# Optimization experiments

Hardware: AMD Instinct MI355X
Metric: run time of the kernel (lower is better)

The kernel has to match this reference:

```python
import jax, jax.numpy as jnp
import numpy as np

T, B, N, GH, GW, ENC, H, D, TH = 16, 512, 8192, 3, 13, 128, 4, 32, 64
G = GH * GW          # 39 social grid cells
EMB = H * D          # 128 = n_head * att_out
SCALE = 1.0 / np.sqrt(ENC).astype(np.float32)
LN_EPS = 1e-5


def lstm(x, Wih, Whh, bih, bhh):
    # x: [T, Batch, in] -> hidden states [T, Batch, ENC]; torch gate order i,f,g,o
    n = x.shape[1]
    h0 = jnp.zeros((n, ENC), x.dtype)

    def step(carry, xt):
        h, c = carry
        g = xt @ Wih.T + bih + h @ Whh.T + bhh
        i, f, gg, o = jnp.split(g, 4, axis=-1)
        c = jax.nn.sigmoid(f) * c + jax.nn.sigmoid(i) * jnp.tanh(gg)
        h = jax.nn.sigmoid(o) * jnp.tanh(c)
        return (h, c), h

    _, hs = jax.lax.scan(step, (h0, h0), x)
    return hs


def glu(x, Wa, ba, Wg, bg):
    return (x @ Wa.T + ba) * jax.nn.sigmoid(x @ Wg.T + bg)


def layer_norm(x, g, b):
    m = jnp.mean(x, -1, keepdims=True)
    v = jnp.var(x, -1, keepdims=True)
    return (x - m) * jax.lax.rsqrt(v + LN_EPS) * g + b


def setup_inputs():
    key = jax.random.key(0)
    ks = jax.random.split(key, 40)

    def rn(i, sh, s=1.0):
        return jax.random.normal(ks[i], sh, jnp.float32) * s

    inp = {
        'hist': rn(0, (T, B, 2)), 'nbrs': rn(1, (T, N, 2)),
        'va': rn(2, (T, B, 2)), 'nbrsva': rn(3, (T, N, 2)),
        'lane': jnp.zeros((T, B, 1), jnp.float32),
        'nbrslane': jnp.zeros((T, N, 1), jnp.float32),
        'cls': rn(4, (T, B, 1)), 'nbrscls': rn(5, (T, N, 1)),
    }
    # boolean social-grid mask with exactly N true cells (cell-level, full enc dim)
    rng = np.random.default_rng(0)
    flat = np.zeros(B * G, bool)
    flat[rng.permutation(B * G)[:N]] = True
    inp['mask'] = jnp.asarray(np.broadcast_to(flat.reshape(B, GH, GW, 1), (B, GH, GW, ENC)))

    s = 0.05
    inp.update({
        'W1': rn(6, (TH, 5), s), 'b1': jnp.zeros((TH,), jnp.float32),
        'Wih': rn(7, (4 * ENC, TH), s), 'Whh': rn(8, (4 * ENC, ENC), s),
        'bih': jnp.zeros((4 * ENC,), jnp.float32), 'bhh': jnp.zeros((4 * ENC,), jnp.float32),
        'Wq': rn(9, (EMB, ENC), s), 'bq': jnp.zeros((EMB,), jnp.float32),
        'Wk': rn(10, (EMB, ENC), s), 'bk': jnp.zeros((EMB,), jnp.float32),
        'Wv': rn(11, (EMB, ENC), s), 'bv': jnp.zeros((EMB,), jnp.float32),
        'Wg1a': rn(12, (ENC, EMB), s), 'bg1a': jnp.zeros((ENC,), jnp.float32),
        'Wg1g': rn(13, (ENC, EMB), s), 'bg1g': jnp.zeros((ENC,), jnp.float32),
        'Wqt': rn(14, (EMB, ENC), s), 'bqt': jnp.zeros((EMB,), jnp.float32),
        'Wkt': rn(15, (EMB, ENC), s), 'bkt': jnp.zeros((EMB,), jnp.float32),
        'Wvt': rn(16, (EMB, ENC), s), 'bvt': jnp.zeros((EMB,), jnp.float32),
        'Wg2a': rn(17, (ENC, EMB), s), 'bg2a': jnp.zeros((ENC,), jnp.float32),
        'Wg2g': rn(18, (ENC, EMB), s), 'bg2g': jnp.zeros((ENC,), jnp.float32),
        'ln_g': jnp.ones((ENC,), jnp.float32), 'ln_b': jnp.zeros((ENC,), jnp.float32),
    })
    return inp


def reference(hist, nbrs, mask, va, nbrsva, lane, nbrslane, cls, nbrscls,
              W1, b1, Wih, Whh, bih, bhh, Wq, bq, Wk, bk, Wv, bv,
              Wg1a, bg1a, Wg1g, bg1g, Wqt, bqt, Wkt, bkt, Wvt, bvt,
              Wg2a, bg2a, Wg2g, bg2g, ln_g, ln_b):
    # f_length == 5 branch
    hist_in = jnp.concatenate((hist, cls, va), -1)        # [T,B,5]
    nbrs_in = jnp.concatenate((nbrs, nbrscls, nbrsva), -1)  # [T,N,5]

    hist_enc = jax.nn.elu(hist_in @ W1.T + b1)
    hist_h = lstm(hist_enc, Wih, Whh, bih, bhh)           # [T,B,ENC]
    hist_hidden = jnp.transpose(hist_h, (1, 0, 2))        # [B,T,ENC]

    nbrs_enc = jax.nn.elu(nbrs_in @ W1.T + b1)
    nbrs_h = lstm(nbrs_enc, Wih, Whh, bih, bhh)           # [T,N,ENC]

    # masked_scatter: fill true grid cells (row-major over B*G) with neighbor states
    cell = mask[:, :, :, 0].reshape(B * G)                # [B*G] bool
    idx = jnp.cumsum(cell.astype(jnp.int32)) - 1          # position among true cells
    gathered = nbrs_h[:, jnp.clip(idx, 0, N - 1), :]      # [T,B*G,ENC]
    soc = jnp.where(cell[None, :, None], gathered, 0.0).reshape(T, B, G, ENC)

    # spatial multi-head attention (each timestep attends over its own grid)
    q = (hist_hidden @ Wq.T + bq).reshape(B, T, H, D)
    k = (soc @ Wk.T + bk).reshape(T, B, G, H, D)
    v = (soc @ Wv.T + bv).reshape(T, B, G, H, D)
    a = jax.nn.softmax(jnp.einsum('bthd,tbghd->bthg', q, k) * SCALE, -1)
    spa = jnp.einsum('bthg,tbghd->bthd', a, v).reshape(B, T, EMB)
    spa = glu(spa, Wg1a, bg1a, Wg1g, bg1g)

    values = layer_norm(hist_hidden + spa, ln_g, ln_b)    # [B,T,ENC]

    # temporal multi-head attention over T
    qt = (values @ Wqt.T + bqt).reshape(B, T, H, D)
    kt = (values @ Wkt.T + bkt).reshape(B, T, H, D)
    vt = (values @ Wvt.T + bvt).reshape(B, T, H, D)
    at = jax.nn.softmax(jnp.einsum('bthd,bshd->bhts', qt, kt) * SCALE, -1)
    tmp = jnp.einsum('bhts,bshd->bthd', at, vt).reshape(B, T, EMB)
    tmp = glu(tmp, Wg2a, bg2a, Wg2g, bg2g)

    # use_spatial=True
    return layer_norm(hist_hidden + spa + tmp, ln_g, ln_b)
```

## Files before the change

### kernel.cpp

```cpp
#include <hip/hip_runtime.h>
#include <math.h>

#define T_ 16
#define B_ 512
#define N_ 8192
#define G_ 39
#define ENC_ 128
#define TH_ 64
#define MROWS 8704
#define GATE 512
#define KCAT 192
#define SCALE_ 0.08838834764831845f
#define LNEPS 1e-5f
#define NBLK 136

typedef short bf16x8 __attribute__((ext_vector_type(8)));
typedef float f32x4  __attribute__((ext_vector_type(4)));

__device__ __forceinline__ float sigm(float x){ return 1.0f/(1.0f+expf(-x)); }
__device__ __forceinline__ float rcpf(float x){ return __builtin_amdgcn_rcpf(x); }
__device__ __forceinline__ float sigm_f(float x){ return rcpf(1.0f + __expf(-x)); }
__device__ __forceinline__ float tanh_f(float x){ return 1.0f - 2.0f*rcpf(__expf(2.0f*x) + 1.0f); }
__device__ __forceinline__ unsigned short f2bf(float f){
  unsigned int u = __float_as_uint(f);
  unsigned int r = u + 0x7FFFu + ((u>>16)&1u);
  return (unsigned short)(r>>16);
}
__device__ __forceinline__ float bf2f(unsigned short h){
  return __uint_as_float(((unsigned int)h)<<16);
}

__global__ __launch_bounds__(256) void k_prep(
    const float* __restrict__ Wih, const float* __restrict__ Whh,
    const float* __restrict__ bih, const float* __restrict__ bhh,
    const float* __restrict__ Wk,  const float* __restrict__ bk,
    const float* __restrict__ Wv,  const float* __restrict__ bv,
    const float* __restrict__ Wq,
    const float* __restrict__ Wqt, const float* __restrict__ bqt,
    const float* __restrict__ Wkt, const float* __restrict__ bkt,
    const float* __restrict__ Wvt, const float* __restrict__ bvt,
    const float* __restrict__ Wg1a, const float* __restrict__ bg1a,
    const float* __restrict__ Wg1g, const float* __restrict__ bg1g,
    const float* __restrict__ Wg2a, const float* __restrict__ bg2a,
    const float* __restrict__ Wg2g, const float* __restrict__ bg2g,
    unsigned short* __restrict__ WcatB, float* __restrict__ biasg,
    unsigned short* __restrict__ WkvB,  float* __restrict__ bkv,
    unsigned short* __restrict__ WqB,
    unsigned short* __restrict__ WqktB, float* __restrict__ bqkt,
    unsigned short* __restrict__ Wg1B,  float* __restrict__ bg1,
    unsigned short* __restrict__ Wg2B,  float* __restrict__ bg2)
{
  int i = blockIdx.x*256 + threadIdx.x;
  if (i < GATE*KCAT) {
    int n = i / KCAT, k = i % KCAT;
    WcatB[i] = f2bf((k < TH_) ? Wih[n*TH_ + k] : Whh[n*ENC_ + (k - TH_)]);
  }
  if (i < GATE) biasg[i] = bih[i] + bhh[i];
  if (i < 2*ENC_*ENC_) {
    int n = i >> 7, k = i & 127;
    WkvB[i] = f2bf((n < ENC_) ? Wk[n*ENC_ + k] : Wv[(n-ENC_)*ENC_ + k]);
    Wg1B[i] = f2bf((n < ENC_) ? Wg1a[n*ENC_ + k] : Wg1g[(n-ENC_)*ENC_ + k]);
    Wg2B[i] = f2bf((n < ENC_) ? Wg2a[n*ENC_ + k] : Wg2g[(n-ENC_)*ENC_ + k]);
  }
  if (i < 2*ENC_) {
    bkv[i] = (i < ENC_) ? bk[i] : bv[i-ENC_];
    bg1[i] = (i < ENC_) ? bg1a[i] : bg1g[i-ENC_];
    bg2[i] = (i < ENC_) ? bg2a[i] : bg2g[i-ENC_];
  }
  if (i < ENC_*ENC_) WqB[i] = f2bf(Wq[i]);
  if (i < 3*ENC_*ENC_) {
    int n = i >> 7, k = i & 127;
    float w = (n < ENC_) ? Wqt[n*ENC_ + k] : (n < 2*ENC_) ? Wkt[(n-ENC_)*ENC_ + k]
                                                          : Wvt[(n-2*ENC_)*ENC_ + k];
    WqktB[i] = f2bf(w);
  }
  if (i < 3*ENC_) bqkt[i] = (i < ENC_) ? bqt[i] : (i < 2*ENC_) ? bkt[i-ENC_] : bvt[i-2*ENC_];
}

__device__ __forceinline__ int cellval(const unsigned char* m, long cell, int w) {
  long byte = cell * 128L * w;
  if (w == 1) return m[byte] != 0;
  if (w == 2) return *(const unsigned short*)(m + byte) != 0;
  if (w == 4) return *(const unsigned int*)(m + byte) != 0;
  return *(const unsigned long long*)(m + byte) != 0ULL;
}
__device__ __forceinline__ int cellconsist(const unsigned char* m, long cell, int w) {
  long byte = cell * 128L * w;
  if (w == 1) { unsigned char v = m[byte];
    for (int j = 1; j < 8; ++j) if (m[byte + j] != v) return 0; return 1; }
  if (w == 2) { unsigned short v = *(const unsigned short*)(m + byte);
    for (int j = 1; j < 8; ++j) if (*(const unsigned short*)(m + byte + 2L*j) != v) return 0; return 1; }
  if (w == 4) { unsigned int v = *(const unsigned int*)(m + byte);
    for (int j = 1; j < 8; ++j) if (*(const unsigned int*)(m + byte + 4L*j) != v) return 0; return 1; }
  unsigned long long v = *(const unsigned long long*)(m + byte);
  for (int j = 1; j < 8; ++j) if (*(const unsigned long long*)(m + byte + 8L*j) != v) return 0; return 1;
}

__global__ void k_detect(const unsigned char* __restrict__ mask, int* __restrict__ wsel)
{
  __shared__ int bad;
  int tid = threadIdx.x;
  int chosen = 0;
  for (int w = 1; w <= 8 && !chosen; w <<= 1) {
    if (tid == 0) bad = 0;
    __syncthreads();
    int ok = 1;
    for (int c = tid; c < 512; c += 256) ok &= cellconsist(mask, c, w);
    if (!ok) bad = 1;
    __syncthreads();
    if (!bad) chosen = w;
    __syncthreads();
  }
  if (tid == 0) *wsel = chosen ? chosen : 1;
}

__global__ void k_count(const unsigned char* __restrict__ mask,
                        const int* __restrict__ wsel, int* __restrict__ bcnt)
{
  __shared__ int sc[256];
  int tid = threadIdx.x;
  long cell = (long)blockIdx.x*256 + tid;
  sc[tid] = cellval(mask, cell, *wsel);
  __syncthreads();
  for (int off = 128; off; off >>= 1) {
    if (tid < off) sc[tid] += sc[tid + off];
    __syncthreads();
  }
  if (tid == 0) bcnt[blockIdx.x] = sc[0];
}

__global__ void k_fill(const unsigned char* __restrict__ mask,
                       const int* __restrict__ wsel, const int* __restrict__ bcnt,
                       int* __restrict__ nidx)
{
  __shared__ int sc[256];
  int tid = threadIdx.x, blk = blockIdx.x;
  long cell = (long)blk*256 + tid;
  int on = cellval(mask, cell, *wsel);
  sc[tid] = on;
  __syncthreads();
  for (int off = 1; off < 256; off <<= 1) {
    int v = (tid >= off) ? sc[tid - off] : 0;
    __syncthreads();
    sc[tid] += v;
    __syncthreads();
  }
  int base = 0;
  for (int i = 0; i < blk; ++i) base += bcnt[i];
  nidx[cell] = on ? (base + sc[tid] - 1) : -1;
}

struct AP {
  const float *hist, *cls, *va, *nbrs, *nbrscls, *nbrsva;
  const float *W1, *b1;
  const unsigned short *Wcat, *Wkv, *Wq;
  const float *biasg, *bkv, *bq;
  float *hh;
  float *qbuf;
  unsigned short *knvB;
  unsigned short *Hsp;
  float *csp;
  int c0, tch;
};

__global__ __launch_bounds__(512, 2) void k_lstm(AP p)
{
  __shared__ unsigned short Hl[2*64*128];
  __shared__ unsigned short Xl[64*64];
  __shared__ float finl[16][64][5];

  const int tid = threadIdx.x;
  const int w = tid >> 6, l = tid & 63;
  const int lr = l & 15, lk = (l >> 4) * 8, lq = (l >> 4) * 4;
  const int bi = blockIdx.x, bm = bi * 64;
  const bool ish = (bi < 8);

  bf16x8 wg[4][6];
  #pragma unroll
  for (int g = 0; g < 4; ++g)
    #pragma unroll
    for (int ks = 0; ks < 6; ++ks)
      wg[g][ks] = *(const bf16x8*)(p.Wcat + (long)(g*128 + w*16 + lr)*KCAT + ks*32 + lk);

  const int ch = w*16 + lr;
  const float bgi = p.biasg[ch], bgf = p.biasg[128+ch],
              bgg = p.biasg[256+ch], bgo = p.biasg[384+ch];

  const float w1c0 = p.W1[l*5+0], w1c1 = p.W1[l*5+1], w1c2 = p.W1[l*5+2],
              w1c3 = p.W1[l*5+3], w1c4 = p.W1[l*5+4], b1c = p.b1[l];

  for (int idx = tid; idx < p.tch*320; idx += 512) {
    int t4 = idx / 320, rem = idx - t4*320;
    int row = rem / 5, f = rem - row*5;
    long r = ish ? ((long)(p.c0 + t4)*B_ + bm + row) : ((long)(p.c0 + t4)*N_ + (bm - B_) + row);
    const float* ph = ish ? p.hist : p.nbrs;
    const float* pc = ish ? p.cls  : p.nbrscls;
    const float* pv = ish ? p.va   : p.nbrsva;
    finl[t4][row][f] = (f < 2) ? ph[r*2 + f] : (f == 2) ? pc[r] : pv[r*2 + (f-3)];
  }

  float creg[4][4];
  if (p.c0 == 0) {
    for (int i = tid; i < 64*128; i += 512) Hl[i] = 0;
    #pragma unroll
    for (int mi = 0; mi < 4; ++mi)
      #pragma unroll
      for (int q = 0; q < 4; ++q) creg[mi][q] = 0.0f;
  } else {
    for (int i = tid; i < 64*128; i += 512) Hl[i] = p.Hsp[(long)bm*128 + i];
    #pragma unroll
    for (int mi = 0; mi < 4; ++mi)
      #pragma unroll
      for (int q = 0; q < 4; ++q) creg[mi][q] = p.csp[((long)bi*512 + tid)*16 + mi*4 + q];
  }
  __syncthreads();

  int cur = 0;
  for (int tl = 0; tl < p.tch; ++tl) {
    int t = p.c0 + tl;
    {
      #pragma unroll
      for (int j = 0; j < 8; ++j) {
        int row = w*8 + j;
        float s = b1c + finl[tl][row][0]*w1c0 + finl[tl][row][1]*w1c1
                      + finl[tl][row][2]*w1c2 + finl[tl][row][3]*w1c3
                      + finl[tl][row][4]*w1c4;
        s = (s > 0.0f) ? s : expm1f(s);
        Xl[row*64 + (l ^ ((row & 7) << 3))] = f2bf(s);
      }
    }
    __syncthreads();
    f32x4 acc[4][4] = {};
    #pragma unroll
    for (int ks = 0; ks < 2; ++ks) {
      bf16x8 a[4];
      #pragma unroll
      for (int mi = 0; mi < 4; ++mi) {
        int row = mi*16 + lr;
        int col = (ks*32 + lk) ^ ((row & 7) << 3);
        a[mi] = *(const bf16x8*)(Xl + row*64 + col);
      }
      #pragma unroll
      for (int g = 0; g < 4; ++g)
        #pragma unroll
        for (int mi = 0; mi < 4; ++mi)
          acc[g][mi] = __builtin_amdgcn_mfma_f32_16x16x32_bf16(a[mi], wg[g][ks], acc[g][mi], 0, 0, 0);
    }
    #pragma unroll
    for (int ks = 0; ks < 4; ++ks) {
      bf16x8 a[4];
      #pragma unroll
      for (int mi = 0; mi < 4; ++mi) {
        int row = mi*16 + lr;
        int col = (ks*32 + lk) ^ ((row & 7) << 3);
        a[mi] = *(const bf16x8*)(Hl + cur*8192 + row*128 + col);
      }
      #pragma unroll
      for (int g = 0; g < 4; ++g)
        #pragma unroll
        for (int mi = 0; mi < 4; ++mi)
          acc[g][mi] = __builtin_amdgcn_mfma_f32_16x16x32_bf16(a[mi], wg[g][2+ks], acc[g][mi], 0, 0, 0);
    }
    int nxt = cur ^ 1;
    #pragma unroll
    for (int mi = 0; mi < 4; ++mi)
      #pragma unroll
      for (int q = 0; q < 4; ++q) {
        int row = mi*16 + lq + q;
        float gi = acc[0][mi][q] + bgi;
        float gf = acc[1][mi][q] + bgf;
        float gg = acc[2][mi][q] + bgg;
        float go = acc[3][mi][q] + bgo;
        float cc = sigm_f(gf)*creg[mi][q] + sigm_f(gi)*tanh_f(gg);
        creg[mi][q] = cc;
        float hv = sigm_f(go)*tanh_f(cc);
        Hl[nxt*8192 + row*128 + (ch ^ ((row & 7) << 3))] = f2bf(hv);
        if (ish) p.hh[((long)(bm + row)*T_ + t)*128 + ch] = hv;
      }
    __syncthreads();
    cur = nxt;
    if (!ish) {
      f32x4 a2[4][2] = {};
      #pragma unroll
      for (int ks = 0; ks < 4; ++ks) {
        bf16x8 a[4];
        #pragma unroll
        for (int mi = 0; mi < 4; ++mi) {
          int row = mi*16 + lr;
          int col = (ks*32 + lk) ^ ((row & 7) << 3);
          a[mi] = *(const bf16x8*)(Hl + cur*8192 + row*128 + col);
        }
        #pragma unroll
        for (int ni = 0; ni < 2; ++ni) {
          bf16x8 b = *(const bf16x8*)(p.Wkv + (long)(w*32 + ni*16 + lr)*128 + ks*32 + lk);
          #pragma unroll
          for (int mi = 0; mi < 4; ++mi)
            a2[mi][ni] = __builtin_amdgcn_mfma_f32_16x16x32_bf16(a[mi], b, a2[mi][ni], 0, 0, 0);
        }
      }
      long nr = bm - B_;
      #pragma unroll
      for (int mi = 0; mi < 4; ++mi)
        #pragma unroll
        for (int ni = 0; ni < 2; ++ni) {
          int c2 = w*32 + ni*16 + lr;
          float bb = p.bkv[c2];
          #pragma unroll
          for (int q = 0; q < 4; ++q)
            p.knvB[((long)tl*N_ + nr + mi*16 + lq + q)*256 + c2] = f2bf(a2[mi][ni][q] + bb);
        }
    } else {
      f32x4 a2[4] = {};
      #pragma unroll
      for (int ks = 0; ks < 4; ++ks) {
        bf16x8 a[4];
        #pragma unroll
        for (int mi = 0; mi < 4; ++mi) {
          int row = mi*16 + lr;
          int col = (ks*32 + lk) ^ ((row & 7) << 3);
          a[mi] = *(const bf16x8*)(Hl + cur*8192 + row*128 + col);
        }
        bf16x8 b = *(const bf16x8*)(p.Wq + (long)(w*16 + lr)*128 + ks*32 + lk);
        #pragma unroll
        for (int mi = 0; mi < 4; ++mi)
          a2[mi] = __builtin_amdgcn_mfma_f32_16x16x32_bf16(a[mi], b, a2[mi], 0, 0, 0);
      }
      float bb = p.bq[ch];
      #pragma unroll
      for (int mi = 0; mi < 4; ++mi)
        #pragma unroll
        for (int q = 0; q < 4; ++q)
          p.qbuf[((long)t*B_ + bm + mi*16 + lq + q)*128 + ch] = a2[mi][q] + bb;
    }
    __syncthreads();
  }
  for (int i = tid; i < 64*128; i += 512) p.Hsp[(long)bm*128 + i] = Hl[cur*8192 + i];
  #pragma unroll
  for (int mi = 0; mi < 4; ++mi)
    #pragma unroll
    for (int q = 0; q < 4; ++q)
      p.csp[((long)bi*512 + tid)*16 + mi*4 + q] = creg[mi][q];
}

__global__ __launch_bounds__(256) void k_attn_sp(
    int c0, int ltch,
    const float* __restrict__ qbuf, const unsigned short* __restrict__ knvB,
    const float* __restrict__ bk, const float* __restrict__ bv,
    const int* __restrict__ nidx, unsigned short* __restrict__ spaB)
{
  int tid = threadIdx.x;
  int w = tid >> 6, l = tid & 63;
  __shared__ int sn[4][G_];
  __shared__ float aw[4][4][40];
  int gwid = blockIdx.x*4 + w;
  int b = gwid >> ltch;
  int tl = gwid & ((1 << ltch) - 1);
  int t = c0 + tl;
  if (l < G_) sn[w][l] = nidx[b*G_ + l];
  __syncthreads();
  float qA = qbuf[((long)t*B_ + b)*128 + l];
  float qB = qbuf[((long)t*B_ + b)*128 + 64 + l];
  for (int g = 0; g < G_; ++g) {
    int ni = sn[w][g];
    const unsigned short* kr = knvB + ((long)tl*N_ + ni)*256;
    float kA = (ni >= 0) ? bf2f(kr[l])      : bk[l];
    float kB = (ni >= 0) ? bf2f(kr[64 + l]) : bk[64 + l];
    float pA = qA*kA, pB = qB*kB;
    pA += __shfl_xor(pA, 16); pA += __shfl_xor(pA, 8); pA += __shfl_xor(pA, 4);
    pA += __shfl_xor(pA, 2);  pA += __shfl_xor(pA, 1);
    pB += __shfl_xor(pB, 16); pB += __shfl_xor(pB, 8); pB += __shfl_xor(pB, 4);
    pB += __shfl_xor(pB, 2);  pB += __shfl_xor(pB, 1);
    if ((l & 31) == 0) {
      int hb = l >> 5;
      aw[w][hb][g]     = pA * SCALE_;
      aw[w][2+hb][g]   = pB * SCALE_;
    }
  }
  __syncthreads();
  int hA = l >> 5, hB = 2 + (l >> 5);
  float mxA = -1e30f, mxB = -1e30f;
  for (int g = 0; g < G_; ++g) {
    mxA = fmaxf(mxA, aw[w][hA][g]);
    mxB = fmaxf(mxB, aw[w][hB][g]);
  }
  float sA = 0.f, sB = 0.f, oA = 0.f, oB = 0.f;
  for (int g = 0; g < G_; ++g) {
    int ni = sn[w][g];
    const unsigned short* vr = knvB + ((long)tl*N_ + ni)*256 + 128;
    float vA = (ni >= 0) ? bf2f(vr[l])      : bv[l];
    float vB = (ni >= 0) ? bf2f(vr[64 + l]) : bv[64 + l];
    float eA = expf(aw[w][hA][g] - mxA);
    float eB = expf(aw[w][hB][g] - mxB);
    sA += eA; sB += eB; oA += eA*vA; oB += eB*vB;
  }
  spaB[((long)b*T_ + t)*128 + l]      = f2bf(oA / sA);
  spaB[((long)b*T_ + t)*128 + 64 + l] = f2bf(oB / sB);
}

__global__ __launch_bounds__(256) void k_gemm_bf16(
    const unsigned short* __restrict__ A, int lda,
    const unsigned short* __restrict__ W, int ldw,
    const float* __restrict__ bias,
    float* __restrict__ C, int ldc, int K)
{
  int tid = threadIdx.x;
  int w = tid >> 6, l = tid & 63;
  int lr = l & 15, lk = (l >> 4) * 8, lq = (l >> 4) * 4;
  int bm = blockIdx.x * 64;
  int bn = blockIdx.y * 128 + w * 32;
  f32x4 acc[4][2] = {};
  for (int k0 = 0; k0 < K; k0 += 32) {
    bf16x8 a[4], b[2];
    #pragma unroll
    for (int mi = 0; mi < 4; ++mi)
      a[mi] = *(const bf16x8*)(A + (long)(bm + mi*16 + lr)*lda + k0 + lk);
    #pragma unroll
    for (int ni = 0; ni < 2; ++ni)
      b[ni] = *(const bf16x8*)(W + (long)(bn + ni*16 + lr)*ldw + k0 + lk);
    #pragma unroll
    for (int mi = 0; mi < 4; ++mi)
      #pragma unroll
      for (int ni = 0; ni < 2; ++ni)
        acc[mi][ni] = __builtin_amdgcn_mfma_f32_16x16x32_bf16(a[mi], b[ni], acc[mi][ni], 0, 0, 0);
  }
  #pragma unroll
  for (int mi = 0; mi < 4; ++mi)
    #pragma unroll
    for (int ni = 0; ni < 2; ++ni) {
      int col = bn + ni*16 + lr;
      float bb = bias[col];
      #pragma unroll
      for (int q = 0; q < 4; ++q)
        C[(long)(bm + mi*16 + lq + q)*ldc + col] = acc[mi][ni][q] + bb;
    }
}

__global__ __launch_bounds__(256) void k_gemm_bf16o(
    const unsigned short* __restrict__ A, int lda,
    const unsigned short* __restrict__ W, int ldw,
    const float* __restrict__ bias,
    unsigned short* __restrict__ C, int ldc, int K)
{
  int tid = threadIdx.x;
  int w = tid >> 6, l = tid & 63;
  int lr = l & 15, lk = (l >> 4) * 8, lq = (l >> 4) * 4;
  int bm = blockIdx.x * 64;
  int bn = blockIdx.y * 128 + w * 32;
  f32x4 acc[4][2] = {};
  for (int k0 = 0; k0 < K; k0 += 32) {
    bf16x8 a[4], b[2];
    #pragma unroll
    for (int mi = 0; mi < 4; ++mi)
      a[mi] = *(const bf16x8*)(A + (long)(bm + mi*16 + lr)*lda + k0 + lk);
    #pragma unroll
    for (int ni = 0; ni < 2; ++ni)
      b[ni] = *(const bf16x8*)(W + (long)(bn + ni*16 + lr)*ldw + k0 + lk);
    #pragma unroll
    for (int mi = 0; mi < 4; ++mi)
      #pragma unroll
      for (int ni = 0; ni < 2; ++ni)
        acc[mi][ni] = __builtin_amdgcn_mfma_f32_16x16x32_bf16(a[mi], b[ni], acc[mi][ni], 0, 0, 0);
  }
  #pragma unroll
  for (int mi = 0; mi < 4; ++mi)
    #pragma unroll
    for (int ni = 0; ni < 2; ++ni) {
      int col = bn + ni*16 + lr;
      float bb = bias[col];
      #pragma unroll
      for (int q = 0; q < 4; ++q)
        C[(long)(bm + mi*16 + lq + q)*ldc + col] = f2bf(acc[mi][ni][q] + bb);
    }
}

__global__ __launch_bounds__(256) void k_glu_addln(
    const float* __restrict__ t12, const float* __restrict__ res,
    const float* __restrict__ lg, const float* __restrict__ lb,
    float* __restrict__ sum_out, unsigned short* __restrict__ ln_bf16,
    float* __restrict__ ln_f32)
{
  int gtid = blockIdx.x*256 + threadIdx.x;
  int r = gtid >> 6;
  int l = threadIdx.x & 63;
  if (r >= B_*T_) return;
  long b4 = (long)r*256, b2 = (long)r*128;
  float xA = res[b2 + l]      + t12[b4 + l]      * sigm(t12[b4 + 128 + l]);
  float xB = res[b2 + 64 + l] + t12[b4 + 64 + l] * sigm(t12[b4 + 192 + l]);
  if (sum_out) { sum_out[b2 + l] = xA; sum_out[b2 + 64 + l] = xB; }
  float s = xA + xB, s2 = xA*xA + xB*xB;
  #pragma unroll
  for (int off = 32; off; off >>= 1) { s += __shfl_xor(s, off); s2 += __shfl_xor(s2, off); }
  float mean = s * (1.0f/128.0f);
  float var  = s2 * (1.0f/128.0f) - mean*mean;
  float inv  = rsqrtf(var + LNEPS);
  float oA = (xA - mean)*inv*lg[l]      + lb[l];
  float oB = (xB - mean)*inv*lg[64 + l] + lb[64 + l];
  if (ln_bf16) { ln_bf16[b2 + l] = f2bf(oA); ln_bf16[b2 + 64 + l] = f2bf(oB); }
  if (ln_f32)  { ln_f32[b2 + l] = oA;        ln_f32[b2 + 64 + l] = oB; }
}

__global__ __launch_bounds__(128) void k_attn_t(
    const unsigned short* __restrict__ qkt, unsigned short* __restrict__ out)
{
  int b = blockIdx.x, tid = threadIdx.x;
  __shared__ float sq[16][128], sk[16][128], sv[16][128];
  __shared__ float sc[16][4][16];
  for (int i = tid; i < T_*ENC_; i += 128) {
    int tt = i >> 7, j = i & 127;
    long a = ((long)b*T_ + tt)*384;
    sq[tt][j] = bf2f(qkt[a + j]);
    sk[tt][j] = bf2f(qkt[a + 128 + j]);
    sv[tt][j] = bf2f(qkt[a + 256 + j]);
  }
  __syncthreads();
  for (int e = tid; e < 1024; e += 128) {
    int t = e >> 6, s = (e >> 2) & 15, h2 = e & 3;
    float pp = 0.0f;
    #pragma unroll
    for (int d2 = 0; d2 < 32; ++d2) pp += sq[t][h2*32 + d2] * sk[s][h2*32 + d2];
    sc[t][h2][s] = pp * SCALE_;
  }
  __syncthreads();
  if (tid < 64) {
    int t = tid >> 2, h2 = tid & 3;
    float mx = -1e30f;
    for (int s = 0; s < 16; ++s) mx = fmaxf(mx, sc[t][h2][s]);
    float sum = 0.0f;
    for (int s = 0; s < 16; ++s) { float e2 = expf(sc[t][h2][s] - mx); sc[t][h2][s] = e2; sum += e2; }
    float inv = 1.0f / sum;
    for (int s = 0; s < 16; ++s) sc[t][h2][s] *= inv;
  }
  __syncthreads();
  int h2 = tid >> 5, d2 = tid & 31;
  for (int t = 0; t < 16; ++t) {
    float acc = 0.0f;
    for (int s = 0; s < 16; ++s) acc += sc[t][h2][s] * sv[s][h2*32 + d2];
    out[((long)b*T_ + t)*128 + tid] = f2bf(acc);
  }
}

extern "C" void kernel_launch(void* const* d_in, const int* in_sizes, int n_in,
                              void* d_out, int out_size, void* d_ws, size_t ws_size,
                              hipStream_t stream)
{
  const float* hist    = (const float*)d_in[0];
  const float* nbrs    = (const float*)d_in[1];
  const float* va      = (const float*)d_in[2];
  const float* nbrsva  = (const float*)d_in[3];
  const float* cls     = (const float*)d_in[6];
  const float* nbrscls = (const float*)d_in[7];
  const unsigned char* mask = (const unsigned char*)d_in[8];
  const float* W1  = (const float*)d_in[9];
  const float* b1  = (const float*)d_in[10];
  const float* Wih = (const float*)d_in[11];
  const float* Whh = (const float*)d_in[12];
  const float* bih = (const float*)d_in[13];
  const float* bhh = (const float*)d_in[14];
  const float* Wq  = (const float*)d_in[15];
  const float* bq  = (const float*)d_in[16];
  const float* Wk  = (const float*)d_in[17];
  const float* bk  = (const float*)d_in[18];
  const float* Wv  = (const float*)d_in[19];
  const float* bv  = (const float*)d_in[20];
  const float* Wg1a = (const float*)d_in[21];
  const float* bg1a = (const float*)d_in[22];
  const float* Wg1g = (const float*)d_in[23];
  const float* bg1g = (const float*)d_in[24];
  const float* Wqt = (const float*)d_in[25];
  const float* bqt = (const float*)d_in[26];
  const float* Wkt = (const float*)d_in[27];
  const float* bkt = (const float*)d_in[28];
  const float* Wvt = (const float*)d_in[29];
  const float* bvt = (const float*)d_in[30];
  const float* Wg2a = (const float*)d_in[31];
  const float* bg2a = (const float*)d_in[32];
  const float* Wg2g = (const float*)d_in[33];
  const float* bg2g = (const float*)d_in[34];
  const float* ln_g = (const float*)d_in[35];
  const float* ln_b = (const float*)d_in[36];

  size_t fixed = 0;
  {
    size_t items[] = {
      (size_t)GATE*KCAT*2, (size_t)GATE*4, (size_t)2*ENC_*ENC_*2, (size_t)2*ENC_*4,
      (size_t)ENC_*ENC_*2, (size_t)3*ENC_*ENC_*2, (size_t)3*ENC_*4,
      (size_t)2*ENC_*ENC_*2, (size_t)2*ENC_*4, (size_t)2*ENC_*ENC_*2, (size_t)2*ENC_*4,
      (size_t)B_*T_*ENC_*4,
      (size_t)T_*B_*ENC_*4,
      (size_t)MROWS*ENC_*2,
      (size_t)NBLK*512*16*4,
      (size_t)B_*T_*ENC_*2,
      (size_t)B_*T_*2*ENC_*4,
      (size_t)B_*T_*ENC_*4,
      (size_t)B_*T_*ENC_*2,
      (size_t)B_*T_*3*ENC_*2,
      (size_t)B_*T_*ENC_*2,
      (size_t)B_*G_*4, (size_t)78*4, (size_t)4
    };
    for (size_t v : items) fixed += (v + 255) & ~(size_t)255;
  }
  int tch = 16, ltch = 4;
  while (tch > 4 && fixed + ((size_t)tch*N_*256*2 + 255) > ws_size) { tch >>= 1; ltch--; }

  char* base = (char*)d_ws;
  size_t off = 0;
  auto alloc = [&](size_t bytes) { char* r = base + off; off = (off + bytes + 255) & ~(size_t)255; return r; };
  unsigned short* WcatB = (unsigned short*)alloc(GATE*KCAT*2);
  float*          biasg = (float*)alloc(GATE*4);
  unsigned short* WkvB  = (unsigned short*)alloc(2*ENC_*ENC_*2);
  float*          bkv   = (float*)alloc(2*ENC_*4);
  unsigned short* WqB   = (unsigned short*)alloc(ENC_*ENC_*2);
  unsigned short* WqktB = (unsigned short*)alloc(3*ENC_*ENC_*2);
  float*          bqkt  = (float*)alloc(3*ENC_*4);
  unsigned short* Wg1B  = (unsigned short*)alloc(2*ENC_*ENC_*2);
  float*          bg1   = (float*)alloc(2*ENC_*4);
  unsigned short* Wg2B  = (unsigned short*)alloc(2*ENC_*ENC_*2);
  float*          bg2   = (float*)alloc(2*ENC_*4);
  float*          hh    = (float*)alloc((size_t)B_*T_*ENC_*4);
  float*          qbuf  = (float*)alloc((size_t)T_*B_*ENC_*4);
  unsigned short* Hsp   = (unsigned short*)alloc((size_t)MROWS*ENC_*2);
  float*          csp   = (float*)alloc((size_t)NBLK*512*16*4);
  unsigned short* spaB  = (unsigned short*)alloc((size_t)B_*T_*ENC_*2);
  float*          t12   = (float*)alloc((size_t)B_*T_*2*ENC_*4);
  float*          S1    = (float*)alloc((size_t)B_*T_*ENC_*4);
  unsigned short* valsB = (unsigned short*)alloc((size_t)B_*T_*ENC_*2);
  unsigned short* qktB  = (unsigned short*)alloc((size_t)B_*T_*3*ENC_*2);
  unsigned short* atoB  = (unsigned short*)alloc((size_t)B_*T_*ENC_*2);
  int*            nidx  = (int*)alloc((size_t)B_*G_*4);
  int*            bcnt  = (int*)alloc(78*4);
  int*            wsel  = (int*)alloc(4);
  unsigned short* knvB  = (unsigned short*)alloc((size_t)tch*N_*256*2);

  k_prep<<<384, 256, 0, stream>>>(
      Wih, Whh, bih, bhh, Wk, bk, Wv, bv, Wq,
      Wqt, bqt, Wkt, bkt, Wvt, bvt,
      Wg1a, bg1a, Wg1g, bg1g, Wg2a, bg2a, Wg2g, bg2g,
      WcatB, biasg, WkvB, bkv, WqB, WqktB, bqkt, Wg1B, bg1, Wg2B, bg2);
  k_detect<<<1, 256, 0, stream>>>(mask, wsel);
  k_count<<<78, 256, 0, stream>>>(mask, wsel, bcnt);
  k_fill<<<78, 256, 0, stream>>>(mask, wsel, bcnt, nidx);

  AP ap;
  ap.hist = hist; ap.cls = cls; ap.va = va;
  ap.nbrs = nbrs; ap.nbrscls = nbrscls; ap.nbrsva = nbrsva;
  ap.W1 = W1; ap.b1 = b1;
  ap.Wcat = WcatB; ap.Wkv = WkvB; ap.Wq = WqB;
  ap.biasg = biasg; ap.bkv = bkv; ap.bq = bq;
  ap.hh = hh; ap.qbuf = qbuf; ap.knvB = knvB; ap.Hsp = Hsp; ap.csp = csp;
  ap.tch = tch;
  for (int c0 = 0; c0 < T_; c0 += tch) {
    ap.c0 = c0;
    k_lstm<<<NBLK, 512, 0, stream>>>(ap);
    k_attn_sp<<<(B_*tch)/4, 256, 0, stream>>>(c0, ltch, qbuf, knvB, bk, bv, nidx, spaB);
  }

  k_gemm_bf16<<<dim3((B_*T_)/64, 2), 256, 0, stream>>>(spaB, 128, Wg1B, 128, bg1, t12, 256, 128);
  k_glu_addln<<<(B_*T_*64)/256, 256, 0, stream>>>(t12, hh, ln_g, ln_b, S1, valsB, nullptr);
  k_gemm_bf16o<<<dim3((B_*T_)/64, 3), 256, 0, stream>>>(valsB, 128, WqktB, 128, bqkt, qktB, 384, 128);
  k_attn_t<<<B_, 128, 0, stream>>>(qktB, atoB);
  k_gemm_bf16<<<dim3((B_*T_)/64, 2), 256, 0, stream>>>(atoB, 128, Wg2B, 128, bg2, t12, 256, 128);
  k_glu_addln<<<(B_*T_*64)/256, 256, 0, stream>>>(t12, S1, ln_g, ln_b, nullptr, nullptr, (float*)d_out);
}
```

Measured before the change: 310.6 us.

## Fold K/V projections into query side and precompute encoder for all timesteps

Spatial attention no longer projects every neighbour hidden state to K and V. The query is multiplied by per-head block-diagonal Wk once per (b,t), and attention runs over raw bf16 neighbour hidden states. Wv is applied after aggregation, with per-head weighted hidden sums fed through a block-diagonal GEMM. The input encoder moves to a separate kernel that writes bf16 features for all timesteps, so the LSTM runs in one launch without chunking or state spill. The cost is storing all neighbour hidden states (T*N*128 bf16), LSTM weights read from global each step instead of held in registers, and occupancy lowered to one block per CU.

```diff
diff --git a/kernel.cpp b/kernel.cpp
--- a/kernel.cpp
+++ b/kernel.cpp
@@ -33,8 +33,7 @@
 __global__ __launch_bounds__(256) void k_prep(
     const float* __restrict__ Wih, const float* __restrict__ Whh,
     const float* __restrict__ bih, const float* __restrict__ bhh,
-    const float* __restrict__ Wk,  const float* __restrict__ bk,
-    const float* __restrict__ Wv,  const float* __restrict__ bv,
+    const float* __restrict__ Wk,  const float* __restrict__ Wv,
     const float* __restrict__ Wq,
     const float* __restrict__ Wqt, const float* __restrict__ bqt,
     const float* __restrict__ Wkt, const float* __restrict__ bkt,
@@ -44,8 +43,9 @@
     const float* __restrict__ Wg2a, const float* __restrict__ bg2a,
     const float* __restrict__ Wg2g, const float* __restrict__ bg2g,
     unsigned short* __restrict__ WcatB, float* __restrict__ biasg,
-    unsigned short* __restrict__ WkvB,  float* __restrict__ bkv,
     unsigned short* __restrict__ WqB,
+    unsigned short* __restrict__ WkD,  unsigned short* __restrict__ WvD,
+    float* __restrict__ zero512,
     unsigned short* __restrict__ WqktB, float* __restrict__ bqkt,
     unsigned short* __restrict__ Wg1B,  float* __restrict__ bg1,
     unsigned short* __restrict__ Wg2B,  float* __restrict__ bg2)
@@ -56,18 +56,27 @@
     WcatB[i] = f2bf((k < TH_) ? Wih[n*TH_ + k] : Whh[n*ENC_ + (k - TH_)]);
   }
   if (i < GATE) biasg[i] = bih[i] + bhh[i];
+  if (i < ENC_*ENC_) WqB[i] = f2bf(Wq[i]);
+  if (i < 512*128) {
+    int r = i >> 7, dc = i & 127;
+    int h = r >> 7, e = r & 127;
+    WkD[i] = ((dc >> 5) == h) ? f2bf(Wk[dc*128 + e]) : (unsigned short)0;
+  }
+  if (i < 128*512) {
+    int r = i >> 9, kk = i & 511;
+    int hp = kk >> 7, e = kk & 127;
+    WvD[i] = (hp == (r >> 5)) ? f2bf(Wv[r*128 + e]) : (unsigned short)0;
+  }
+  if (i < 512) zero512[i] = 0.0f;
   if (i < 2*ENC_*ENC_) {
     int n = i >> 7, k = i & 127;
-    WkvB[i] = f2bf((n < ENC_) ? Wk[n*ENC_ + k] : Wv[(n-ENC_)*ENC_ + k]);
     Wg1B[i] = f2bf((n < ENC_) ? Wg1a[n*ENC_ + k] : Wg1g[(n-ENC_)*ENC_ + k]);
     Wg2B[i] = f2bf((n < ENC_) ? Wg2a[n*ENC_ + k] : Wg2g[(n-ENC_)*ENC_ + k]);
   }
   if (i < 2*ENC_) {
-    bkv[i] = (i < ENC_) ? bk[i] : bv[i-ENC_];
     bg1[i] = (i < ENC_) ? bg1a[i] : bg1g[i-ENC_];
     bg2[i] = (i < ENC_) ? bg2a[i] : bg2g[i-ENC_];
   }
-  if (i < ENC_*ENC_) WqB[i] = f2bf(Wq[i]);
   if (i < 3*ENC_*ENC_) {
     int n = i >> 7, k = i & 127;
     float w = (n < ENC_) ? Wqt[n*ENC_ + k] : (n < 2*ENC_) ? Wkt[(n-ENC_)*ENC_ + k]
@@ -150,24 +159,39 @@
   nidx[cell] = on ? (base + sc[tid] - 1) : -1;
 }
 
+__global__ __launch_bounds__(256) void k_encode_all(
+    const float* __restrict__ hist, const float* __restrict__ cls, const float* __restrict__ va,
+    const float* __restrict__ nbrs, const float* __restrict__ nbrscls, const float* __restrict__ nbrsva,
+    const float* __restrict__ W1, const float* __restrict__ b1,
+    unsigned short* __restrict__ XencB)
+{
+  int i = blockIdx.x*256 + threadIdx.x;
+  int t = blockIdx.y;
+  int o = i & 63, m = i >> 6;
+  float in0, in1, in2, in3, in4;
+  if (m < B_) {
+    int r = t*B_ + m;
+    in0 = hist[r*2]; in1 = hist[r*2+1]; in2 = cls[r]; in3 = va[r*2]; in4 = va[r*2+1];
+  } else {
+    int r = t*N_ + (m - B_);
+    in0 = nbrs[r*2]; in1 = nbrs[r*2+1]; in2 = nbrscls[r]; in3 = nbrsva[r*2]; in4 = nbrsva[r*2+1];
+  }
+  const float* w = W1 + o*5;
+  float s = b1[o] + in0*w[0] + in1*w[1] + in2*w[2] + in3*w[3] + in4*w[4];
+  XencB[((long)t*MROWS + m)*64 + o] = f2bf((s > 0.0f) ? s : expm1f(s));
+}
+
 struct AP {
-  const float *hist, *cls, *va, *nbrs, *nbrscls, *nbrsva;
-  const float *W1, *b1;
-  const unsigned short *Wcat, *Wkv, *Wq;
-  const float *biasg, *bkv, *bq;
+  const unsigned short *Xenc, *Wcat, *Wq;
+  const float *biasg, *bq;
   float *hh;
-  float *qbuf;
-  unsigned short *knvB;
-  unsigned short *Hsp;
-  float *csp;
-  int c0, tch;
+  unsigned short *qB;
+  unsigned short *HnB;
 };
 
-__global__ __launch_bounds__(512, 2) void k_lstm(AP p)
+__global__ __launch_bounds__(512, 1) void k_lstm(AP p)
 {
   __shared__ unsigned short Hl[2*64*128];
-  __shared__ unsigned short Xl[64*64];
-  __shared__ float finl[16][64][5];
 
   const int tid = threadIdx.x;
   const int w = tid >> 6, l = tid & 63;
@@ -175,76 +199,42 @@
   const int bi = blockIdx.x, bm = bi * 64;
   const bool ish = (bi < 8);
 
-  bf16x8 wg[4][6];
+  bf16x8 wgh[4][4];
   #pragma unroll
   for (int g = 0; g < 4; ++g)
     #pragma unroll
-    for (int ks = 0; ks < 6; ++ks)
-      wg[g][ks] = *(const bf16x8*)(p.Wcat + (long)(g*128 + w*16 + lr)*KCAT + ks*32 + lk);
+    for (int ks = 0; ks < 4; ++ks)
+      wgh[g][ks] = *(const bf16x8*)(p.Wcat + (long)(g*128 + w*16 + lr)*KCAT + 64 + ks*32 + lk);
 
   const int ch = w*16 + lr;
   const float bgi = p.biasg[ch], bgf = p.biasg[128+ch],
               bgg = p.biasg[256+ch], bgo = p.biasg[384+ch];
-
-  const float w1c0 = p.W1[l*5+0], w1c1 = p.W1[l*5+1], w1c2 = p.W1[l*5+2],
-              w1c3 = p.W1[l*5+3], w1c4 = p.W1[l*5+4], b1c = p.b1[l];
-
-  for (int idx = tid; idx < p.tch*320; idx += 512) {
-    int t4 = idx / 320, rem = idx - t4*320;
-    int row = rem / 5, f = rem - row*5;
-    long r = ish ? ((long)(p.c0 + t4)*B_ + bm + row) : ((long)(p.c0 + t4)*N_ + (bm - B_) + row);
-    const float* ph = ish ? p.hist : p.nbrs;
-    const float* pc = ish ? p.cls  : p.nbrscls;
-    const float* pv = ish ? p.va   : p.nbrsva;
-    finl[t4][row][f] = (f < 2) ? ph[r*2 + f] : (f == 2) ? pc[r] : pv[r*2 + (f-3)];
-  }
-
+  const float bqv = ish ? p.bq[ch] : 0.0f;
+
+  for (int i = tid; i < 64*128; i += 512) Hl[i] = 0;
   float creg[4][4];
-  if (p.c0 == 0) {
-    for (int i = tid; i < 64*128; i += 512) Hl[i] = 0;
-    #pragma unroll
-    for (int mi = 0; mi < 4; ++mi)
-      #pragma unroll
-      for (int q = 0; q < 4; ++q) creg[mi][q] = 0.0f;
-  } else {
-    for (int i = tid; i < 64*128; i += 512) Hl[i] = p.Hsp[(long)bm*128 + i];
-    #pragma unroll
-    for (int mi = 0; mi < 4; ++mi)
-      #pragma unroll
-      for (int q = 0; q < 4; ++q) creg[mi][q] = p.csp[((long)bi*512 + tid)*16 + mi*4 + q];
-  }
+  #pragma unroll
+  for (int mi = 0; mi < 4; ++mi)
+    #pragma unroll
+    for (int q = 0; q < 4; ++q) creg[mi][q] = 0.0f;
   __syncthreads();
 
   int cur = 0;
-  for (int tl = 0; tl < p.tch; ++tl) {
-    int t = p.c0 + tl;
-    {
-      #pragma unroll
-      for (int j = 0; j < 8; ++j) {
-        int row = w*8 + j;
-        float s = b1c + finl[tl][row][0]*w1c0 + finl[tl][row][1]*w1c1
-                      + finl[tl][row][2]*w1c2 + finl[tl][row][3]*w1c3
-                      + finl[tl][row][4]*w1c4;
-        s = (s > 0.0f) ? s : expm1f(s);
-        Xl[row*64 + (l ^ ((row & 7) << 3))] = f2bf(s);
-      }
-    }
-    __syncthreads();
+  for (int t = 0; t < T_; ++t) {
     f32x4 acc[4][4] = {};
     #pragma unroll
     for (int ks = 0; ks < 2; ++ks) {
       bf16x8 a[4];
       #pragma unroll
-      for (int mi = 0; mi < 4; ++mi) {
-        int row = mi*16 + lr;
-        int col = (ks*32 + lk) ^ ((row & 7) << 3);
-        a[mi] = *(const bf16x8*)(Xl + row*64 + col);
-      }
-      #pragma unroll
-      for (int g = 0; g < 4; ++g)
+      for (int mi = 0; mi < 4; ++mi)
+        a[mi] = *(const bf16x8*)(p.Xenc + ((long)t*MROWS + bm + mi*16 + lr)*64 + ks*32 + lk);
+      #pragma unroll
+      for (int g = 0; g < 4; ++g) {
+        bf16x8 b = *(const bf16x8*)(p.Wcat + (long)(g*128 + w*16 + lr)*KCAT + ks*32 + lk);
         #pragma unroll
         for (int mi = 0; mi < 4; ++mi)
-          acc[g][mi] = __builtin_amdgcn_mfma_f32_16x16x32_bf16(a[mi], wg[g][ks], acc[g][mi], 0, 0, 0);
+          acc[g][mi] = __builtin_amdgcn_mfma_f32_16x16x32_bf16(a[mi], b, acc[g][mi], 0, 0, 0);
+      }
     }
     #pragma unroll
     for (int ks = 0; ks < 4; ++ks) {
@@ -259,7 +249,7 @@
       for (int g = 0; g < 4; ++g)
         #pragma unroll
         for (int mi = 0; mi < 4; ++mi)
-          acc[g][mi] = __builtin_amdgcn_mfma_f32_16x16x32_bf16(a[mi], wg[g][2+ks], acc[g][mi], 0, 0, 0);
+          acc[g][mi] = __builtin_amdgcn_mfma_f32_16x16x32_bf16(a[mi], wgh[g][ks], acc[g][mi], 0, 0, 0);
     }
     int nxt = cur ^ 1;
     #pragma unroll
@@ -279,122 +269,95 @@
       }
     __syncthreads();
     cur = nxt;
-    if (!ish) {
-      f32x4 a2[4][2] = {};
+    if (ish) {
+      f32x4 a2[4] = {};
       #pragma unroll
       for (int ks = 0; ks < 4; ++ks) {
-        bf16x8 a[4];
+        bf16x8 b = *(const bf16x8*)(p.Wq + (long)(w*16 + lr)*128 + ks*32 + lk);
         #pragma unroll
         for (int mi = 0; mi < 4; ++mi) {
           int row = mi*16 + lr;
           int col = (ks*32 + lk) ^ ((row & 7) << 3);
-          a[mi] = *(const bf16x8*)(Hl + cur*8192 + row*128 + col);
-        }
-        #pragma unroll
-        for (int ni = 0; ni < 2; ++ni) {
-          bf16x8 b = *(const bf16x8*)(p.Wkv + (long)(w*32 + ni*16 + lr)*128 + ks*32 + lk);
-          #pragma unroll
-          for (int mi = 0; mi < 4; ++mi)
-            a2[mi][ni] = __builtin_amdgcn_mfma_f32_16x16x32_bf16(a[mi], b, a2[mi][ni], 0, 0, 0);
+          bf16x8 a = *(const bf16x8*)(Hl + cur*8192 + row*128 + col);
+          a2[mi] = __builtin_amdgcn_mfma_f32_16x16x32_bf16(a, b, a2[mi], 0, 0, 0);
         }
       }
-      long nr = bm - B_;
-      #pragma unroll
-      for (int mi = 0; mi < 4; ++mi)
-        #pragma unroll
-        for (int ni = 0; ni < 2; ++ni) {
-          int c2 = w*32 + ni*16 + lr;
-          float bb = p.bkv[c2];
-          #pragma unroll
-          for (int q = 0; q < 4; ++q)
-            p.knvB[((long)tl*N_ + nr + mi*16 + lq + q)*256 + c2] = f2bf(a2[mi][ni][q] + bb);
-        }
-    } else {
-      f32x4 a2[4] = {};
-      #pragma unroll
-      for (int ks = 0; ks < 4; ++ks) {
-        bf16x8 a[4];
-        #pragma unroll
-        for (int mi = 0; mi < 4; ++mi) {
-          int row = mi*16 + lr;
-          int col = (ks*32 + lk) ^ ((row & 7) << 3);
-          a[mi] = *(const bf16x8*)(Hl + cur*8192 + row*128 + col);
-        }
-        bf16x8 b = *(const bf16x8*)(p.Wq + (long)(w*16 + lr)*128 + ks*32 + lk);
-        #pragma unroll
-        for (int mi = 0; mi < 4; ++mi)
-          a2[mi] = __builtin_amdgcn_mfma_f32_16x16x32_bf16(a[mi], b, a2[mi], 0, 0, 0);
-      }
-      float bb = p.bq[ch];
       #pragma unroll
       for (int mi = 0; mi < 4; ++mi)
         #pragma unroll
         for (int q = 0; q < 4; ++q)
-          p.qbuf[((long)t*B_ + bm + mi*16 + lq + q)*128 + ch] = a2[mi][q] + bb;
+          p.qB[((long)t*B_ + bm + mi*16 + lq + q)*128 + ch] = f2bf(a2[mi][q] + bqv);
+    } else {
+      for (int e = tid; e < 64*16; e += 512) {
+        int r = e >> 4, j = e & 15;
+        int src = cur*8192 + r*128 + ((j*8) ^ ((r & 7) << 3));
+        *(bf16x8*)(p.HnB + ((long)t*N_ + (bm - B_) + r)*128 + j*8) =
+            *(const bf16x8*)(Hl + src);
+      }
     }
-    __syncthreads();
-  }
-  for (int i = tid; i < 64*128; i += 512) p.Hsp[(long)bm*128 + i] = Hl[cur*8192 + i];
-  #pragma unroll
-  for (int mi = 0; mi < 4; ++mi)
-    #pragma unroll
-    for (int q = 0; q < 4; ++q)
-      p.csp[((long)bi*512 + tid)*16 + mi*4 + q] = creg[mi][q];
-}
-
-__global__ __launch_bounds__(256) void k_attn_sp(
-    int c0, int ltch,
-    const float* __restrict__ qbuf, const unsigned short* __restrict__ knvB,
-    const float* __restrict__ bk, const float* __restrict__ bv,
-    const int* __restrict__ nidx, unsigned short* __restrict__ spaB)
-{
+  }
+}
+
+__global__ __launch_bounds__(128) void k_attn2(
+    const unsigned short* __restrict__ qB,
+    const unsigned short* __restrict__ qWB,
+    const unsigned short* __restrict__ HnB,
+    const float* __restrict__ bk,
+    const int* __restrict__ nidx,
+    unsigned short* __restrict__ hbarB)
+{
+  __shared__ int sn[G_];
+  __shared__ unsigned short hL[G_*128];
+  __shared__ float sgh[G_][4];
+  int blk = blockIdx.x;
+  int b = blk >> 4, t = blk & 15;
   int tid = threadIdx.x;
-  int w = tid >> 6, l = tid & 63;
-  __shared__ int sn[4][G_];
-  __shared__ float aw[4][4][40];
-  int gwid = blockIdx.x*4 + w;
-  int b = gwid >> ltch;
-  int tl = gwid & ((1 << ltch) - 1);
-  int t = c0 + tl;
-  if (l < G_) sn[w][l] = nidx[b*G_ + l];
-  __syncthreads();
-  float qA = qbuf[((long)t*B_ + b)*128 + l];
-  float qB = qbuf[((long)t*B_ + b)*128 + 64 + l];
+  int h = tid >> 5, d = tid & 31;
+  if (tid < G_) sn[tid] = nidx[b*G_ + tid];
+  __syncthreads();
   for (int g = 0; g < G_; ++g) {
-    int ni = sn[w][g];
-    const unsigned short* kr = knvB + ((long)tl*N_ + ni)*256;
-    float kA = (ni >= 0) ? bf2f(kr[l])      : bk[l];
-    float kB = (ni >= 0) ? bf2f(kr[64 + l]) : bk[64 + l];
-    float pA = qA*kA, pB = qB*kB;
-    pA += __shfl_xor(pA, 16); pA += __shfl_xor(pA, 8); pA += __shfl_xor(pA, 4);
-    pA += __shfl_xor(pA, 2);  pA += __shfl_xor(pA, 1);
-    pB += __shfl_xor(pB, 16); pB += __shfl_xor(pB, 8); pB += __shfl_xor(pB, 4);
-    pB += __shfl_xor(pB, 2);  pB += __shfl_xor(pB, 1);
-    if ((l & 31) == 0) {
-      int hb = l >> 5;
-      aw[w][hb][g]     = pA * SCALE_;
-      aw[w][2+hb][g]   = pB * SCALE_;
+    int ni = sn[g];
+    if (ni >= 0) hL[g*128 + tid] = HnB[((long)t*N_ + ni)*128 + tid];
+  }
+  float qel = bf2f(qB[((long)t*B_ + b)*128 + tid]);
+  float qbk = qel * bk[tid];
+  #pragma unroll
+  for (int off = 16; off; off >>= 1) qbk += __shfl_xor(qbk, off);
+  float qw[4];
+  #pragma unroll
+  for (int j = 0; j < 4; ++j)
+    qw[j] = bf2f(qWB[((long)t*B_ + b)*512 + h*128 + d + j*32]);
+  __syncthreads();
+  for (int g = 0; g < G_; ++g) {
+    float s;
+    if (sn[g] >= 0) {
+      float part = 0.0f;
+      #pragma unroll
+      for (int j = 0; j < 4; ++j) part += bf2f(hL[g*128 + d + j*32]) * qw[j];
+      #pragma unroll
+      for (int off = 16; off; off >>= 1) part += __shfl_xor(part, off);
+      s = (part + qbk) * SCALE_;
+    } else {
+      s = qbk * SCALE_;
     }
-  }
-  __syncthreads();
-  int hA = l >> 5, hB = 2 + (l >> 5);
-  float mxA = -1e30f, mxB = -1e30f;
+    if (d == 0) sgh[g][h] = s;
+  }
+  float mx = -1e30f;
+  for (int g = 0; g < G_; ++g) mx = fmaxf(mx, sgh[g][h]);
+  float den = 0.0f;
+  float hb[4] = {0.0f, 0.0f, 0.0f, 0.0f};
   for (int g = 0; g < G_; ++g) {
-    mxA = fmaxf(mxA, aw[w][hA][g]);
-    mxB = fmaxf(mxB, aw[w][hB][g]);
-  }
-  float sA = 0.f, sB = 0.f, oA = 0.f, oB = 0.f;
-  for (int g = 0; g < G_; ++g) {
-    int ni = sn[w][g];
-    const unsigned short* vr = knvB + ((long)tl*N_ + ni)*256 + 128;
-    float vA = (ni >= 0) ? bf2f(vr[l])      : bv[l];
-    float vB = (ni >= 0) ? bf2f(vr[64 + l]) : bv[64 + l];
-    float eA = expf(aw[w][hA][g] - mxA);
-    float eB = expf(aw[w][hB][g] - mxB);
-    sA += eA; sB += eB; oA += eA*vA; oB += eB*vB;
-  }
-  spaB[((long)b*T_ + t)*128 + l]      = f2bf(oA / sA);
-  spaB[((long)b*T_ + t)*128 + 64 + l] = f2bf(oB / sB);
+    float e = expf(sgh[g][h] - mx);
+    den += e;
+    if (sn[g] >= 0) {
+      #pragma unroll
+      for (int j = 0; j < 4; ++j) hb[j] += e * bf2f(hL[g*128 + d + j*32]);
+    }
+  }
+  float inv = 1.0f / den;
+  #pragma unroll
+  for (int j = 0; j < 4; ++j)
+    hbarB[((long)b*T_ + t)*512 + h*128 + d + j*32] = f2bf(hb[j] * inv);
 }
 
 __global__ __launch_bounds__(256) void k_gemm_bf16(
@@ -579,47 +542,27 @@
   const float* ln_g = (const float*)d_in[35];
   const float* ln_b = (const float*)d_in[36];
 
-  size_t fixed = 0;
-  {
-    size_t items[] = {
-      (size_t)GATE*KCAT*2, (size_t)GATE*4, (size_t)2*ENC_*ENC_*2, (size_t)2*ENC_*4,
-      (size_t)ENC_*ENC_*2, (size_t)3*ENC_*ENC_*2, (size_t)3*ENC_*4,
-      (size_t)2*ENC_*ENC_*2, (size_t)2*ENC_*4, (size_t)2*ENC_*ENC_*2, (size_t)2*ENC_*4,
-      (size_t)B_*T_*ENC_*4,
-      (size_t)T_*B_*ENC_*4,
-      (size_t)MROWS*ENC_*2,
-      (size_t)NBLK*512*16*4,
-      (size_t)B_*T_*ENC_*2,
-      (size_t)B_*T_*2*ENC_*4,
-      (size_t)B_*T_*ENC_*4,
-      (size_t)B_*T_*ENC_*2,
-      (size_t)B_*T_*3*ENC_*2,
-      (size_t)B_*T_*ENC_*2,
-      (size_t)B_*G_*4, (size_t)78*4, (size_t)4
-    };
-    for (size_t v : items) fixed += (v + 255) & ~(size_t)255;
-  }
-  int tch = 16, ltch = 4;
-  while (tch > 4 && fixed + ((size_t)tch*N_*256*2 + 255) > ws_size) { tch >>= 1; ltch--; }
-
   char* base = (char*)d_ws;
   size_t off = 0;
   auto alloc = [&](size_t bytes) { char* r = base + off; off = (off + bytes + 255) & ~(size_t)255; return r; };
   unsigned short* WcatB = (unsigned short*)alloc(GATE*KCAT*2);
   float*          biasg = (float*)alloc(GATE*4);
-  unsigned short* WkvB  = (unsigned short*)alloc(2*ENC_*ENC_*2);
-  float*          bkv   = (float*)alloc(2*ENC_*4);
   unsigned short* WqB   = (unsigned short*)alloc(ENC_*ENC_*2);
+  unsigned short* WkD   = (unsigned short*)alloc(512*128*2);
+  unsigned short* WvD   = (unsigned short*)alloc(128*512*2);
+  float*          zero512 = (float*)alloc(512*4);
   unsigned short* WqktB = (unsigned short*)alloc(3*ENC_*ENC_*2);
   float*          bqkt  = (float*)alloc(3*ENC_*4);
   unsigned short* Wg1B  = (unsigned short*)alloc(2*ENC_*ENC_*2);
   float*          bg1   = (float*)alloc(2*ENC_*4);
   unsigned short* Wg2B  = (unsigned short*)alloc(2*ENC_*ENC_*2);
   float*          bg2   = (float*)alloc(2*ENC_*4);
+  unsigned short* XencB = (unsigned short*)alloc((size_t)T_*MROWS*64*2);
   float*          hh    = (float*)alloc((size_t)B_*T_*ENC_*4);
-  float*          qbuf  = (float*)alloc((size_t)T_*B_*ENC_*4);
-  unsigned short* Hsp   = (unsigned short*)alloc((size_t)MROWS*ENC_*2);
-  float*          csp   = (float*)alloc((size_t)NBLK*512*16*4);
+  unsigned short* qB    = (unsigned short*)alloc((size_t)T_*B_*ENC_*2);
+  unsigned short* HnB   = (unsigned short*)alloc((size_t)T_*N_*ENC_*2);
+  unsigned short* qWB   = (unsigned short*)alloc((size_t)T_*B_*512*2);
+  unsigned short* hbarB = (unsigned short*)alloc((size_t)B_*T_*512*2);
   unsigned short* spaB  = (unsigned short*)alloc((size_t)B_*T_*ENC_*2);
   float*          t12   = (float*)alloc((size_t)B_*T_*2*ENC_*4);
   float*          S1    = (float*)alloc((size_t)B_*T_*ENC_*4);
@@ -629,35 +572,34 @@
   int*            nidx  = (int*)alloc((size_t)B_*G_*4);
   int*            bcnt  = (int*)alloc(78*4);
   int*            wsel  = (int*)alloc(4);
-  unsigned short* knvB  = (unsigned short*)alloc((size_t)tch*N_*256*2);
+
+  const int ROWS = B_*T_;
 
   k_prep<<<384, 256, 0, stream>>>(
-      Wih, Whh, bih, bhh, Wk, bk, Wv, bv, Wq,
+      Wih, Whh, bih, bhh, Wk, Wv, Wq,
       Wqt, bqt, Wkt, bkt, Wvt, bvt,
       Wg1a, bg1a, Wg1g, bg1g, Wg2a, bg2a, Wg2g, bg2g,
-      WcatB, biasg, WkvB, bkv, WqB, WqktB, bqkt, Wg1B, bg1, Wg2B, bg2);
+      WcatB, biasg, WqB, WkD, WvD, zero512, WqktB, bqkt, Wg1B, bg1, Wg2B, bg2);
   k_detect<<<1, 256, 0, stream>>>(mask, wsel);
   k_count<<<78, 256, 0, stream>>>(mask, wsel, bcnt);
   k_fill<<<78, 256, 0, stream>>>(mask, wsel, bcnt, nidx);
+  k_encode_all<<<dim3(MROWS*64/256, T_), 256, 0, stream>>>(
+      hist, cls, va, nbrs, nbrscls, nbrsva, W1, b1, XencB);
 
   AP ap;
-  ap.hist = hist; ap.cls = cls; ap.va = va;
-  ap.nbrs = nbrs; ap.nbrscls = nbrscls; ap.nbrsva = nbrsva;
-  ap.W1 = W1; ap.b1 = b1;
-  ap.Wcat = WcatB; ap.Wkv = WkvB; ap.Wq = WqB;
-  ap.biasg = biasg; ap.bkv = bkv; ap.bq = bq;
-  ap.hh = hh; ap.qbuf = qbuf; ap.knvB = knvB; ap.Hsp = Hsp; ap.csp = csp;
-  ap.tch = tch;
-  for (int c0 = 0; c0 < T_; c0 += tch) {
-    ap.c0 = c0;
-    k_lstm<<<NBLK, 512, 0, stream>>>(ap);
-    k_attn_sp<<<(B_*tch)/4, 256, 0, stream>>>(c0, ltch, qbuf, knvB, bk, bv, nidx, spaB);
-  }
-
-  k_gemm_bf16<<<dim3((B_*T_)/64, 2), 256, 0, stream>>>(spaB, 128, Wg1B, 128, bg1, t12, 256, 128);
-  k_glu_addln<<<(B_*T_*64)/256, 256, 0, stream>>>(t12, hh, ln_g, ln_b, S1, valsB, nullptr);
-  k_gemm_bf16o<<<dim3((B_*T_)/64, 3), 256, 0, stream>>>(valsB, 128, WqktB, 128, bqkt, qktB, 384, 128);
+  ap.Xenc = XencB; ap.Wcat = WcatB; ap.Wq = WqB;
+  ap.biasg = biasg; ap.bq = bq;
+  ap.hh = hh; ap.qB = qB; ap.HnB = HnB;
+  k_lstm<<<NBLK, 512, 0, stream>>>(ap);
+
+  k_gemm_bf16o<<<dim3(ROWS/64, 4), 256, 0, stream>>>(qB, 128, WkD, 128, zero512, qWB, 512, 128);
+  k_attn2<<<ROWS, 128, 0, stream>>>(qB, qWB, HnB, bk, nidx, hbarB);
+  k_gemm_bf16o<<<dim3(ROWS/64, 1), 256, 0, stream>>>(hbarB, 512, WvD, 512, bv, spaB, 128, 512);
+
+  k_gemm_bf16<<<dim3(ROWS/64, 2), 256, 0, stream>>>(spaB, 128, Wg1B, 128, bg1, t12, 256, 128);
+  k_glu_addln<<<(ROWS*64)/256, 256, 0, stream>>>(t12, hh, ln_g, ln_b, S1, valsB, nullptr);
+  k_gemm_bf16o<<<dim3(ROWS/64, 3), 256, 0, stream>>>(valsB, 128, WqktB, 128, bqkt, qktB, 384, 128);
   k_attn_t<<<B_, 128, 0, stream>>>(qktB, atoB);
-  k_gemm_bf16<<<dim3((B_*T_)/64, 2), 256, 0, stream>>>(atoB, 128, Wg2B, 128, bg2, t12, 256, 128);
-  k_glu_addln<<<(B_*T_*64)/256, 256, 0, stream>>>(t12, S1, ln_g, ln_b, nullptr, nullptr, (float*)d_out);
-}
+  k_gemm_bf16<<<dim3(ROWS/64, 2), 256, 0, stream>>>(atoB, 128, Wg2B, 128, bg2, t12, 256, 128);
+  k_glu_addln<<<(ROWS*64)/256, 256, 0, stream>>>(t12, S1, ln_g, ln_b, nullptr, nullptr, (float*)d_out);
+}
```

Result: slower. 351.7 us (+13.2%).
